# Kernel optimization log

Hardware: AMD Instinct MI355X
Metric: run time of the kernel (lower is better)

The kernel has to match this reference:

```python
import jax, jax.numpy as jnp
import numpy as np

EPS = 1e-5
K_PATCHES = 5000  # sample_pixels // 16


def _resize_bilinear(x, h, w):
    # matches torch F.interpolate(mode='bilinear', align_corners=False)
    return jax.image.resize(x, (x.shape[0], x.shape[1], h, w), method="bilinear", antialias=False)


def _bn(x, g, b, m, v):
    # eval-mode BatchNorm2d with running stats
    inv = jax.lax.rsqrt(v + EPS)
    return (x - m[None, :, None, None]) * (g * inv)[None, :, None, None] + b[None, :, None, None]


def _conv(x, w):
    return jax.lax.conv_general_dilated(x, w, (1, 1), "VALID",
                                        dimension_numbers=("NCHW", "OIHW", "NCHW"))


def setup_inputs():
    key = jax.random.key(0)
    ks = jax.random.split(key, 14)
    B, Hc, Wc = 2, 512, 512
    pha = jax.random.uniform(ks[0], (B, 1, Hc, Wc), jnp.float32)
    err = jax.random.uniform(ks[1], (B, 1, Hc, Wc), jnp.float32)  # strictly >0 so mask is all-ones
    hid = jax.random.normal(ks[2], (B, 32, Hc, Wc), jnp.float32)

    def conv_w(k, o, i):
        return jax.random.normal(k, (o, i, 3, 3), jnp.float32) * 0.05

    def bn_p(k, c):
        k1, k2 = jax.random.split(k)
        return (1.0 + 0.1 * jax.random.normal(k1, (c,), jnp.float32),
                0.1 * jax.random.normal(k2, (c,), jnp.float32),
                jnp.zeros((c,), jnp.float32), jnp.ones((c,), jnp.float32))

    g1, b1, m1, v1 = bn_p(ks[4], 24)
    g2, b2, m2, v2 = bn_p(ks[6], 16)
    g3, b3, m3, v3 = bn_p(ks[8], 12)
    return dict(pha=pha, err=err, hid=hid,
                w1=conv_w(ks[3], 24, 33), g1=g1, b1=b1, m1=m1, v1=v1,
                w2=conv_w(ks[5], 16, 24), g2=g2, b2=b2, m2=m2, v2=v2,
                w3=conv_w(ks[7], 12, 16), g3=g3, b3=b3, m3=m3, v3=v3,
                w4=conv_w(ks[9], 1, 12),
                b4=0.1 * jax.random.normal(ks[10], (1,), jnp.float32),
                H_full=2048, W_full=2048)


def reference(pha, err, hid, w1, g1, b1, m1, v1, w2, g2, b2, m2, v2,
              w3, g3, b3, m3, v3, w4, b4, H_full, W_full):
    B = pha.shape[0]
    Hh, Wh = H_full // 2, W_full // 2
    Hq, Wq = H_full // 4, W_full // 4

    # --- select_refinement_regions (sampling mode) ---
    err_q = _resize_bilinear(err, Hq, Wq)                      # (B,1,Hq,Wq)
    flat = err_q.reshape(B, -1)
    _, top_idx = jax.lax.top_k(flat, K_PATCHES)                # (B,K)
    ref = jnp.zeros_like(flat).at[jnp.arange(B)[:, None], top_idx].set(1.0)
    ref = ref * (flat > 0).astype(flat.dtype)                  # prevent_oversampling
    ref = ref.reshape(B, 1, Hq, Wq)

    # nonzero(ref) == topk locations here (err is strictly positive)
    bidx = jnp.repeat(jnp.arange(B), K_PATCHES)                # (P,)
    hidx = (top_idx // Wq).reshape(-1)                         # (P,)
    widx = (top_idx % Wq).reshape(-1)                          # (P,)

    # --- crop_patch (unfold-equivalent gather), size=2, padding=3 ---
    x = jnp.concatenate([hid, pha], axis=1)                    # (B,33,Hc,Wc)
    x = _resize_bilinear(x, Hh, Wh)                            # (B,33,Hh,Wh)
    pad, size = 3, 2
    win = size + 2 * pad                                       # 8
    xp = jnp.pad(x, ((0, 0), (0, 0), (pad, pad), (pad, pad)))
    rows = hidx[:, None] * size + jnp.arange(win)              # (P,8)
    cols = widx[:, None] * size + jnp.arange(win)              # (P,8)
    patches = xp[bidx[:, None, None], :, rows[:, :, None], cols[:, None, :]]  # (P,8,8,33)
    patches = patches.transpose(0, 3, 1, 2)                    # (P,33,8,8)

    # --- small conv stack ---
    y = jax.nn.relu(_bn(_conv(patches, w1), g1, b1, m1, v1))   # (P,24,6,6)
    y = jax.nn.relu(_bn(_conv(y, w2), g2, b2, m2, v2))         # (P,16,4,4)
    y = jnp.repeat(jnp.repeat(y, 2, axis=2), 2, axis=3)        # nearest -> (P,16,8,8)
    y = jax.nn.relu(_bn(_conv(y, w3), g3, b3, m3, v3))         # (P,12,6,6)
    y = _conv(y, w4) + b4[None, :, None, None]                 # (P,1,4,4)

    # --- replace_patch (scatter_nd of 4x4 blocks into full-res pha) ---
    pha_full = _resize_bilinear(pha, H_full, W_full)           # (B,1,H,W)
    pr = hidx[:, None, None] * 4 + jnp.arange(4)[None, :, None]  # (P,4,1)
    pc = widx[:, None, None] * 4 + jnp.arange(4)[None, None, :]  # (P,1,4)
    pha_full = pha_full.at[bidx[:, None, None], 0, pr, pc].set(y[:, 0])
    return pha_full, ref
```

## Files before the change

kernel.cpp:

```cpp
#include <hip/hip_runtime.h>
#include <stdint.h>

#define K_SEL 5000
#define NQ    262144
#define NB    2

#define BIAS_OFF 38912
#define W4_OFF   39424
#define ST_OFF   40960
#define XT_OFF   135168
#define XT_BYTES ((size_t)NB * NQ * 40 * 2)
#define WS_NEED  (XT_OFF + XT_BYTES)

#define WS_HIST  16
#define WS_SEL   2064
#define WS_EQ    12064
#define EQ_CAP   4096
#define WS_BCNT  20480

typedef _Float16 f16x8 __attribute__((ext_vector_type(8)));
typedef _Float16 f16x4 __attribute__((ext_vector_type(4)));
typedef float    f32x4 __attribute__((ext_vector_type(4)));
#define MFMA16(a,b,c) __builtin_amdgcn_mfma_f32_16x16x32_f16(a,b,c,0,0,0)

__global__ void prep_kernel(const float* __restrict__ w1, const float* __restrict__ g1,
                            const float* __restrict__ b1, const float* __restrict__ m1,
                            const float* __restrict__ v1,
                            const float* __restrict__ w2, const float* __restrict__ g2,
                            const float* __restrict__ b2, const float* __restrict__ m2,
                            const float* __restrict__ v2,
                            const float* __restrict__ w3, const float* __restrict__ g3,
                            const float* __restrict__ b3, const float* __restrict__ m3,
                            const float* __restrict__ v3,
                            const float* __restrict__ w4, const float* __restrict__ b4,
                            char* __restrict__ ws) {
    _Float16* wf = (_Float16*)ws;
    float* bias = (float*)(ws + BIAS_OFF);
    float* w4r  = (float*)(ws + W4_OFF);
    uint32_t* st = (uint32_t*)(ws + ST_OFF);
    int tid = threadIdx.x;
    for (int t = blockIdx.x * 256 + tid; t < 38 * 512; t += 64 * 256) {
        int frag = t >> 9, li = (t >> 3) & 63, j = t & 7;
        int lo = li & 15, hi = li >> 4;
        float val = 0.f;
        if (frag < 18) {
            int ky = frag / 6, r = frag % 6, kx = r >> 1, mt = r & 1;
            int oc = mt * 16 + lo, ci = hi * 8 + j;
            if (oc < 24) val = w1[((oc * 33 + ci) * 3 + ky) * 3 + kx] * g1[oc] * rsqrtf(v1[oc] + 1e-5f);
        } else if (frag < 27) {
            int f = frag - 18, ky = f / 3, kt = f % 3;
            int oc = lo, k = kt * 32 + hi * 8 + j;
            if (k < 72) {
                int kx = k / 24, ci = k % 24;
                val = w2[((oc * 24 + ci) * 3 + ky) * 3 + kx] * g2[oc] * rsqrtf(v2[oc] + 1e-5f);
            }
        } else if (frag < 36) {
            int s = frag - 27, ky = s / 3, kx = s % 3;
            int oc = lo, ci = hi * 8 + j;
            if (oc < 12 && ci < 16) val = w3[((oc * 16 + ci) * 3 + ky) * 3 + kx] * g3[oc] * rsqrtf(v3[oc] + 1e-5f);
        } else {
            int mt = frag - 36, oc = mt * 16 + lo, tap = hi * 8 + j;
            if (oc < 24 && tap < 9)
                val = w1[((oc * 33 + 32) * 3 + tap / 3) * 3 + tap % 3] * g1[oc] * rsqrtf(v1[oc] + 1e-5f);
        }
        wf[t] = (_Float16)val;
    }
    if (blockIdx.x == 0) {
        if (tid < 53) {
            float v;
            if (tid < 24)      { float sc = g1[tid] * rsqrtf(v1[tid] + 1e-5f); v = b1[tid] - m1[tid] * sc; }
            else if (tid < 40) { int c = tid - 24; float sc = g2[c] * rsqrtf(v2[c] + 1e-5f); v = b2[c] - m2[c] * sc; }
            else if (tid < 52) { int c = tid - 40; float sc = g3[c] * rsqrtf(v3[c] + 1e-5f); v = b3[c] - m3[c] * sc; }
            else v = b4[0];
            bias[tid] = v;
        }
        if (tid < 144) { int t9 = tid / 16, ci = tid % 16; w4r[tid] = (ci < 12) ? w4[ci * 9 + t9] : 0.f; }
        for (int i = tid; i < WS_HIST + 4 * 512; i += 256) st[i] = 0u;
    }
}

__device__ __forceinline__ void chain_scan(const uint32_t* __restrict__ st, int b, int nrounds,
                                           uint32_t* pref_out, uint32_t* rem_out) {
    int lane = threadIdx.x & 63;
    uint32_t pref = 0u, rem = K_SEL;
    for (int r = 0; r < nrounds; r++) {
        const uint32_t* hist = st + WS_HIST + r * 512 + b * 256;
        int binbase = 255 - 4 * lane;
        uint32_t hv0 = hist[binbase], hv1 = hist[binbase - 1],
                 hv2 = hist[binbase - 2], hv3 = hist[binbase - 3];
        uint32_t p = hv0 + hv1 + hv2 + hv3;
        uint32_t cum = p;
        for (int o = 1; o < 64; o <<= 1) {
            uint32_t n = __shfl_up(cum, o);
            if (lane >= o) cum += n;
        }
        unsigned long long bal = __ballot(cum >= rem);
        int first = __ffsll(bal) - 1;
        uint32_t acc = cum - p;
        uint32_t hv[4] = {hv0, hv1, hv2, hv3};
        int ch = binbase;
        for (int q = 0; q < 4; q++) {
            if (acc + hv[q] >= rem) { ch = binbase - q; break; }
            acc += hv[q];
        }
        uint32_t chosen = (uint32_t)__shfl((int)ch, first);
        uint32_t nrem   = (uint32_t)__shfl((int)(rem - acc), first);
        pref |= chosen << (24 - 8 * r);
        rem = nrem;
    }
    *pref_out = pref;
    *rem_out = rem;
}

__device__ __forceinline__ void tu_work(int tb, const float* __restrict__ hid,
                                        const float* __restrict__ pha,
                                        _Float16* __restrict__ xt,
                                        float* __restrict__ out) {
    int tid = threadIdx.x;
    if (tb < 2048) {
        int t = tb * 256 + tid;
        int b = t >> 18, i = t & (NQ - 1);
        _Float16 v[40];
#pragma unroll
        for (int c = 0; c < 32; c++)
            v[c] = (_Float16)hid[((size_t)(b * 32 + c)) * NQ + i];
        v[32] = (_Float16)pha[(size_t)b * NQ + i];
#pragma unroll
        for (int c = 33; c < 40; c++) v[c] = (_Float16)0.f;
        _Float16* dst = xt + (size_t)t * 40;
#pragma unroll
        for (int q = 0; q < 5; q++) *(f16x8*)(dst + q * 8) = *(const f16x8*)(v + q * 8);
    } else {
        int t = (tb - 2048) * 256 + tid;
        int xq = t & 511;
        int rest = t >> 9;
        int oy = rest & 2047;
        int b  = rest >> 11;
        const float* src = pha + (size_t)b * NQ;
        float sy = oy * 0.25f - 0.375f;
        sy = fminf(fmaxf(sy, 0.0f), 511.0f);
        int y0 = (int)sy; int y1i = min(y0 + 1, 511);
        float fy = sy - (float)y0;
        float rv[4];
#pragma unroll
        for (int j = 0; j < 4; j++) {
            int ox = xq * 4 + j;
            float sx = ox * 0.25f - 0.375f;
            sx = fminf(fmaxf(sx, 0.0f), 511.0f);
            int x0 = (int)sx; int x1i = min(x0 + 1, 511);
            float fx = sx - (float)x0;
            float v00 = src[y0 * 512 + x0],  v01 = src[y0 * 512 + x1i];
            float v10 = src[y1i * 512 + x0], v11 = src[y1i * 512 + x1i];
            rv[j] = v00 * (1.f - fy) * (1.f - fx) + v01 * (1.f - fy) * fx
                  + v10 * fy * (1.f - fx)         + v11 * fy * fx;
        }
        float4 r4 = make_float4(rv[0], rv[1], rv[2], rv[3]);
        *reinterpret_cast<float4*>(out + (size_t)b * 4194304 + (size_t)oy * 2048 + xq * 4) = r4;
    }
}

__global__ void upsample_kernel(const float* __restrict__ pha, float* __restrict__ out) {
    int t = blockIdx.x * 256 + threadIdx.x;
    int xq = t & 511;
    int rest = t >> 9;
    int oy = rest & 2047;
    int b  = rest >> 11;
    const float* src = pha + (size_t)b * NQ;
    float sy = oy * 0.25f - 0.375f;
    sy = fminf(fmaxf(sy, 0.0f), 511.0f);
    int y0 = (int)sy; int y1i = min(y0 + 1, 511);
    float fy = sy - (float)y0;
    float rv[4];
#pragma unroll
    for (int j = 0; j < 4; j++) {
        int ox = xq * 4 + j;
        float sx = ox * 0.25f - 0.375f;
        sx = fminf(fmaxf(sx, 0.0f), 511.0f);
        int x0 = (int)sx; int x1i = min(x0 + 1, 511);
        float fx = sx - (float)x0;
        float v00 = src[y0 * 512 + x0],  v01 = src[y0 * 512 + x1i];
        float v10 = src[y1i * 512 + x0], v11 = src[y1i * 512 + x1i];
        rv[j] = v00 * (1.f - fy) * (1.f - fx) + v01 * (1.f - fy) * fx
              + v10 * fy * (1.f - fx)         + v11 * fy * fx;
    }
    float4 r4 = make_float4(rv[0], rv[1], rv[2], rv[3]);
    *reinterpret_cast<float4*>(out + (size_t)b * 4194304 + (size_t)oy * 2048 + xq * 4) = r4;
}

__global__ void hist_kernel(const float* __restrict__ err, uint32_t* st, int round,
                            const float* __restrict__ hid, const float* __restrict__ pha,
                            _Float16* __restrict__ xt, float* __restrict__ out, int tu_base) {
    if (blockIdx.x >= 2048) { tu_work(blockIdx.x - 2048 + tu_base, hid, pha, xt, out); return; }
    __shared__ uint32_t h[256];
    h[threadIdx.x] = 0u;
    int t = blockIdx.x * 256 + threadIdx.x;
    int b = t >> 18;
    uint32_t pref = 0u, rem;
    if (round > 0) chain_scan(st, b, round, &pref, &rem);
    __syncthreads();
    uint32_t bits = __float_as_uint(err[t]);
    int shift = 24 - 8 * round;
    bool match = (round == 0) || ((bits >> (shift + 8)) == (pref >> (shift + 8)));
    if (match) atomicAdd(&h[(bits >> shift) & 255u], 1u);
    __syncthreads();
    uint32_t v = h[threadIdx.x];
    if (v) atomicAdd(&st[WS_HIST + round * 512 + b * 256 + threadIdx.x], v);
}

__global__ void ccount_kernel(const float* __restrict__ err, uint32_t* st,
                              const float* __restrict__ hid, const float* __restrict__ pha,
                              _Float16* __restrict__ xt, float* __restrict__ out, int tu_base) {
    if (blockIdx.x >= 1024) { tu_work(blockIdx.x - 1024 + tu_base, hid, pha, xt, out); return; }
    __shared__ uint32_t wsum[8];
    int blk = blockIdx.x, tid = threadIdx.x;
    int b = blk >> 9, base = (blk & 511) << 9;
    uint32_t T, need;
    chain_scan(st, b, 4, &T, &need);
    if ((blk & 511) == 0 && tid == 0) {
        atomicExch(&st[4 + b], T);
        atomicExch(&st[6 + b], need);
    }
    uint32_t b0 = __float_as_uint(err[b * NQ + base + tid]);
    uint32_t b1 = __float_as_uint(err[b * NQ + base + 256 + tid]);
    unsigned long long m0 = __ballot(b0 > T);
    unsigned long long m1 = __ballot(b1 > T);
    int w = tid >> 6, lane = tid & 63;
    if (lane == 0) { wsum[w] = (uint32_t)__popcll(m0); wsum[4 + w] = (uint32_t)__popcll(m1); }
    __syncthreads();
    if (tid == 0)
        st[WS_BCNT + blk] = wsum[0] + wsum[1] + wsum[2] + wsum[3]
                          + wsum[4] + wsum[5] + wsum[6] + wsum[7];
}

__global__ void cplace_kernel(const float* __restrict__ err, uint32_t* st,
                              float* __restrict__ refout,
                              const float* __restrict__ hid, const float* __restrict__ pha,
                              _Float16* __restrict__ xt, float* __restrict__ out, int tu_base) {
    if (blockIdx.x >= 1024) { tu_work(blockIdx.x - 1024 + tu_base, hid, pha, xt, out); return; }
    __shared__ uint32_t wc[8];
    __shared__ uint32_t red[4];
    int blk = blockIdx.x, tid = threadIdx.x;
    int b = blk >> 9, base = (blk & 511) << 9;
    int w = tid >> 6, lane = tid & 63;
    uint32_t T = st[4 + b];
    uint32_t myp = blk & 511;
    uint32_t c0 = st[WS_BCNT + b * 512 + 2 * tid];
    uint32_t c1 = st[WS_BCNT + b * 512 + 2 * tid + 1];
    uint32_t v = (((uint32_t)(2 * tid) < myp) ? c0 : 0u) + (((uint32_t)(2 * tid + 1) < myp) ? c1 : 0u);
    for (int o = 1; o < 64; o <<= 1) v += __shfl_xor(v, o);
    if (lane == 0) red[w] = v;
    __syncthreads();
    uint32_t blkbase = red[0] + red[1] + red[2] + red[3];
    if (myp == 511 && tid == 0)
        atomicExch(&st[8 + b], blkbase + st[WS_BCNT + b * 512 + 511]);
    int i0 = base + tid, i1 = base + 256 + tid;
    uint32_t b0 = __float_as_uint(err[b * NQ + i0]);
    uint32_t b1 = __float_as_uint(err[b * NQ + i1]);
    bool s0 = b0 > T, s1 = b1 > T;
    unsigned long long m0 = __ballot(s0);
    unsigned long long m1 = __ballot(s1);
    if (lane == 0) { wc[w] = (uint32_t)__popcll(m0); wc[4 + w] = (uint32_t)__popcll(m1); }
    refout[b * NQ + i0] = s0 ? 1.0f : 0.0f;
    refout[b * NQ + i1] = s1 ? 1.0f : 0.0f;
    __syncthreads();
    uint32_t tot0 = wc[0] + wc[1] + wc[2] + wc[3];
    uint32_t pre0 = 0, pre1 = tot0;
    for (int j = 0; j < w; j++) { pre0 += wc[j]; pre1 += wc[4 + j]; }
    unsigned long long lt = (1ull << lane) - 1ull;
    if (s0) {
        uint32_t slot = blkbase + pre0 + (uint32_t)__popcll(m0 & lt);
        if (slot < K_SEL) st[WS_SEL + b * K_SEL + slot] = (uint32_t)i0;
    }
    if (s1) {
        uint32_t slot = blkbase + pre1 + (uint32_t)__popcll(m1 & lt);
        if (slot < K_SEL) st[WS_SEL + b * K_SEL + slot] = (uint32_t)i1;
    }
    if (b0 == T) { uint32_t e = atomicAdd(&st[10 + b], 1u); if (e < EQ_CAP) st[WS_EQ + b * EQ_CAP + e] = (uint32_t)i0; }
    if (b1 == T) { uint32_t e = atomicAdd(&st[10 + b], 1u); if (e < EQ_CAP) st[WS_EQ + b * EQ_CAP + e] = (uint32_t)i1; }
}

__global__ void select_kernel(uint32_t* st, float* __restrict__ refout) {
    __shared__ uint32_t L[EQ_CAP];
    int b = blockIdx.x;
    uint32_t m = st[10 + b]; if (m > EQ_CAP) m = EQ_CAP;
    uint32_t need = st[6 + b];
    uint32_t T = st[4 + b];
    for (uint32_t j = threadIdx.x; j < m; j += blockDim.x) L[j] = st[WS_EQ + b * EQ_CAP + j];
    __syncthreads();
    for (uint32_t j = threadIdx.x; j < m; j += blockDim.x) {
        uint32_t idx = L[j];
        uint32_t rank = 0;
        for (uint32_t q = 0; q < m; q++) rank += (L[q] < idx) ? 1u : 0u;
        if (rank < need) {
            uint32_t slot = atomicAdd(&st[8 + b], 1u);
            if (slot < K_SEL) st[WS_SEL + b * K_SEL + slot] = idx;
            refout[b * NQ + idx] = (T != 0u) ? 1.0f : 0.0f;
        }
    }
}

__device__ __forceinline__ f16x8 ldfrag(const _Float16* wf, int frag, int l) {
    return *(const f16x8*)(wf + frag * 512 + l * 8);
}

template<bool XT>
__global__ __launch_bounds__(128) void patch_kernel(
    const float* __restrict__ hid, const float* __restrict__ pha,
    const _Float16* __restrict__ xt,
    const char* __restrict__ ws, float* __restrict__ out) {
    __shared__ _Float16 xs[64][40];
    __shared__ _Float16 y1n[36][40];
    __shared__ _Float16 pool[64][40];
    __shared__ float pha8[64];
    __shared__ float biasL[56];
    float* y3s = (float*)&y1n[0][0];

    const _Float16* wf = (const _Float16*)ws;
    const float* biasG = (const float*)(ws + BIAS_OFF);
    const float* w4r   = (const float*)(ws + W4_OFF);
    const uint32_t* st = (const uint32_t*)(ws + ST_OFF);

    int tid = threadIdx.x, l = tid & 63, wid = tid >> 6;
    int lo = l & 15, hi = l >> 4;
    int bp = blockIdx.x;
    int b = (bp >= K_SEL) ? 1 : 0;
    int pi = bp - b * K_SEL;
    uint32_t idx = st[WS_SEL + b * K_SEL + pi] & 0x3FFFFu;
    int hq = (int)(idx >> 9), wq = (int)(idx & 511u);

    if (tid < 53) biasL[tid] = biasG[tid];

    int ry = l >> 3, rx = l & 7;
    int hy = hq * 2 + ry - 3, hx = wq * 2 + rx - 3;
    bool inb = ((unsigned)hy < 1024u) && ((unsigned)hx < 1024u);
    float sy = fminf(fmaxf(hy * 0.5f - 0.25f, 0.f), 511.f);
    float sx = fminf(fmaxf(hx * 0.5f - 0.25f, 0.f), 511.f);
    int y0 = (int)sy, x0 = (int)sx;
    int y1c = min(y0 + 1, 511), x1c = min(x0 + 1, 511);
    float fy = sy - (float)y0, fx = sx - (float)x0;
    int o00 = y0 * 512 + x0, o01 = y0 * 512 + x1c, o10 = y1c * 512 + x0, o11 = y1c * 512 + x1c;
    float w00 = (1.f - fy) * (1.f - fx), w01 = (1.f - fy) * fx;
    float w10 = fy * (1.f - fx), w11 = fy * fx;

    _Float16 hv[16];
    if (XT) {
        if (inb) {
            const _Float16* xtb = xt + (size_t)b * NQ * 40 + (size_t)wid * 16;
            const _Float16* p00 = xtb + (size_t)o00 * 40;
            const _Float16* p01 = xtb + (size_t)o01 * 40;
            const _Float16* p10 = xtb + (size_t)o10 * 40;
            const _Float16* p11 = xtb + (size_t)o11 * 40;
            f16x8 a0 = *(const f16x8*)p00, a1 = *(const f16x8*)(p00 + 8);
            f16x8 b0 = *(const f16x8*)p01, b1 = *(const f16x8*)(p01 + 8);
            f16x8 c0 = *(const f16x8*)p10, c1 = *(const f16x8*)(p10 + 8);
            f16x8 d0 = *(const f16x8*)p11, d1 = *(const f16x8*)(p11 + 8);
#pragma unroll
            for (int j = 0; j < 8; j++) {
                hv[j]     = (_Float16)(w00 * (float)a0[j] + w01 * (float)b0[j]
                                     + w10 * (float)c0[j] + w11 * (float)d0[j]);
                hv[j + 8] = (_Float16)(w00 * (float)a1[j] + w01 * (float)b1[j]
                                     + w10 * (float)c1[j] + w11 * (float)d1[j]);
            }
        } else {
#pragma unroll
            for (int c = 0; c < 16; c++) hv[c] = (_Float16)0.f;
        }
    } else {
        const float* hb = hid + ((size_t)b * 32 + wid * 16) * NQ;
#pragma unroll
        for (int c = 0; c < 16; c++) {
            const float* p = hb + (size_t)c * NQ;
            float v = 0.f;
            if (inb) v = p[o00] * w00 + p[o01] * w01 + p[o10] * w10 + p[o11] * w11;
            hv[c] = (_Float16)v;
        }
    }
    f16x8 h0 = {hv[0], hv[1], hv[2], hv[3], hv[4], hv[5], hv[6], hv[7]};
    f16x8 h1 = {hv[8], hv[9], hv[10], hv[11], hv[12], hv[13], hv[14], hv[15]};
    {
        _Float16* xrow = &xs[l][wid * 16];
        *(f16x8*)xrow = h0;
        *((f16x8*)xrow + 1) = h1;
    }
    f16x8 z8 = {(_Float16)0.f, (_Float16)0.f, (_Float16)0.f, (_Float16)0.f,
                (_Float16)0.f, (_Float16)0.f, (_Float16)0.f, (_Float16)0.f};
    if (wid == 1) {
        const float* p = pha + (size_t)b * NQ;
        float v = 0.f;
        if (inb) v = p[o00] * w00 + p[o01] * w01 + p[o10] * w10 + p[o11] * w11;
        pha8[l] = v;
    }
    __syncthreads();

    if (wid == 0) {
        if (l < 48) {
            int py = (l * 43) >> 8, px = l - py * 6;
            _Float16 tap[9];
#pragma unroll
            for (int t = 0; t < 9; t++) {
                int ky = t / 3, kx = t % 3;
                int ip = (py + ky) * 8 + px + kx;
                tap[t] = (_Float16)pha8[ip & 63];
            }
            _Float16* row = &pool[l][0];
            f16x8 r0 = {tap[0], tap[1], tap[2], tap[3], tap[4], tap[5], tap[6], tap[7]};
            f16x8 r1 = z8; r1[0] = tap[8];
            *(f16x8*)row = r0;
            *(f16x8*)(row + 8)  = r1;
            *(f16x8*)(row + 16) = z8;
            *(f16x8*)(row + 24) = z8;
        }
    } else {
        for (int i = l; i < 72; i += 64) {
            *(f16x8*)&y1n[i >> 1][24 + (i & 1) * 8] = z8;
        }
    }
    __syncthreads();

    f32x4 zf = {0.f, 0.f, 0.f, 0.f};
    f32x4 aA0 = zf, aA1 = zf, aB = zf;
    int nA = wid * 16 + lo, nB = 32 + lo;
    int pyA = (nA * 43) >> 8, pxA = nA - pyA * 6;
    int pyB = (nB * 43) >> 8, pxB = nB - pyB * 6;
    {
        f16x8 A0 = ldfrag(wf, 36, l), A1 = ldfrag(wf, 37, l);
        f16x8 BA = *(const f16x8*)&pool[nA][hi * 8];
        f16x8 BB = *(const f16x8*)&pool[nB][hi * 8];
        aA0 = MFMA16(A0, BA, aA0);
        aA1 = MFMA16(A1, BA, aA1);
        aB  = MFMA16(wid ? A1 : A0, BB, aB);
    }
#pragma unroll
    for (int ky = 0; ky < 3; ky++) {
#pragma unroll
        for (int kt = 0; kt < 3; kt++) {
            f16x8 A0 = ldfrag(wf, ky * 6 + kt * 2 + 0, l);
            f16x8 A1 = ldfrag(wf, ky * 6 + kt * 2 + 1, l);
            int rA = ((pyA + ky) * 8 + pxA + kt) & 63;
            int rB = ((pyB + ky) * 8 + pxB + kt) & 63;
            f16x8 BA = *(const f16x8*)&xs[rA][hi * 8];
            f16x8 BB = *(const f16x8*)&xs[rB][hi * 8];
            aA0 = MFMA16(A0, BA, aA0);
            aA1 = MFMA16(A1, BA, aA1);
            aB  = MFMA16(wid ? A1 : A0, BB, aB);
        }
    }
    {
        f32x4 accs[3] = {aA0, aA1, aB};
        int mts[3] = {0, 1, wid};
        int nts[3] = {wid, wid, 2};
#pragma unroll
        for (int f = 0; f < 3; f++) {
            int n = nts[f] * 16 + lo;
            int ocb = mts[f] * 16 + hi * 4;
            if (n < 36 && ocb < 24) {
                f16x4 hh;
                hh[0] = (_Float16)fmaxf(accs[f][0] + biasL[ocb + 0], 0.f);
                hh[1] = (_Float16)fmaxf(accs[f][1] + biasL[ocb + 1], 0.f);
                hh[2] = (_Float16)fmaxf(accs[f][2] + biasL[ocb + 2], 0.f);
                hh[3] = (_Float16)fmaxf(accs[f][3] + biasL[ocb + 3], 0.f);
                *(f16x4*)&y1n[n][ocb] = hh;
            }
        }
    }
    __syncthreads();

    if (wid == 0) {
        f32x4 a2 = zf;
        int qy = lo >> 2, qx = lo & 3;
#pragma unroll
        for (int ky = 0; ky < 3; ky++) {
#pragma unroll
            for (int kt = 0; kt < 3; kt++) {
                f16x8 A = ldfrag(wf, 18 + ky * 3 + kt, l);
                int k = kt * 32 + hi * 8;
                const _Float16* bptr;
                if (k < 72) {
                    int kx = k / 24, ci0 = k - kx * 24;
                    bptr = &y1n[(qy + ky) * 6 + qx + kx][ci0];
                } else {
                    bptr = &y1n[0][24];
                }
                f16x8 B = *(const f16x8*)bptr;
                a2 = MFMA16(A, B, a2);
            }
        }
        int ocb = hi * 4;
        f16x4 hh;
        hh[0] = (_Float16)fmaxf(a2[0] + biasL[24 + ocb + 0], 0.f);
        hh[1] = (_Float16)fmaxf(a2[1] + biasL[24 + ocb + 1], 0.f);
        hh[2] = (_Float16)fmaxf(a2[2] + biasL[24 + ocb + 2], 0.f);
        hh[3] = (_Float16)fmaxf(a2[3] + biasL[24 + ocb + 3], 0.f);
#pragma unroll
        for (int dy = 0; dy < 2; dy++)
#pragma unroll
            for (int dx = 0; dx < 2; dx++) {
                int row = (2 * qy + dy) * 8 + 2 * qx + dx;
                *(f16x4*)&pool[row][ocb] = hh;
            }
    } else {
        *(f16x8*)&pool[l][16] = z8;
        *(f16x8*)&pool[l][24] = z8;
    }
    __syncthreads();

    f32x4 aC = zf, aD = zf;
    int nC = wid * 16 + lo, nD = 32 + lo;
    int pyC = (nC * 43) >> 8, pxC = nC - pyC * 6;
    int pyD = (nD * 43) >> 8, pxD = nD - pyD * 6;
#pragma unroll
    for (int s = 0; s < 9; s++) {
        int ky = s / 3, kx = s % 3;
        f16x8 A = ldfrag(wf, 27 + s, l);
        f16x8 BC = *(const f16x8*)&pool[((pyC + ky) * 8 + pxC + kx) & 63][hi * 8];
        aC = MFMA16(A, BC, aC);
        if (wid) {
            f16x8 BD = *(const f16x8*)&pool[((pyD + ky) * 8 + pxD + kx) & 63][hi * 8];
            aD = MFMA16(A, BD, aD);
        }
    }
    __syncthreads();
    {
        int ocb = hi * 4;
        f32x4 accs[2] = {aC, aD};
        int nts[2] = {wid, 2};
        int cnt = wid ? 2 : 1;
        for (int f = 0; f < cnt; f++) {
            int n = nts[f] * 16 + lo;
            if (n < 36) {
                f32x4 v;
#pragma unroll
                for (int r = 0; r < 4; r++) {
                    float bb = (ocb + r < 12) ? biasL[40 + ocb + r] : 0.f;
                    float x = accs[f][r] + bb;
                    v[r] = (ocb + r < 12) ? fmaxf(x, 0.f) : 0.f;
                }
                *(f32x4*)&y3s[n * 16 + ocb] = v;
            }
        }
    }
    __syncthreads();

    if (wid == 0) {
        int r4 = lo >> 2, c4 = lo & 3, cig = hi;
        float acc = 0.f;
#pragma unroll
        for (int t = 0; t < 9; t++) {
            int ky = t / 3, kx = t % 3;
            const f32x4 xv = *(const f32x4*)&y3s[((r4 + ky) * 6 + c4 + kx) * 16 + cig * 4];
            const f32x4 wv = *(const f32x4*)(w4r + t * 16 + cig * 4);
            acc += xv[0] * wv[0] + xv[1] * wv[1] + xv[2] * wv[2] + xv[3] * wv[3];
        }
        acc += __shfl_xor(acc, 32);
        acc += __shfl_xor(acc, 16);
        if (l < 16) {
            out[(size_t)b * 4194304 + (size_t)(hq * 4 + r4) * 2048 + (wq * 4 + c4)] = acc + biasL[52];
        }
    }
}

extern "C" void kernel_launch(void* const* d_in, const int* in_sizes, int n_in,
                              void* d_out, int out_size, void* d_ws, size_t ws_size,
                              hipStream_t stream) {
    const float* pha = (const float*)d_in[0];
    const float* err = (const float*)d_in[1];
    const float* hid = (const float*)d_in[2];
    const float* w1  = (const float*)d_in[3];
    const float* g1  = (const float*)d_in[4];
    const float* bb1 = (const float*)d_in[5];
    const float* m1  = (const float*)d_in[6];
    const float* v1  = (const float*)d_in[7];
    const float* w2  = (const float*)d_in[8];
    const float* g2  = (const float*)d_in[9];
    const float* bb2 = (const float*)d_in[10];
    const float* m2  = (const float*)d_in[11];
    const float* v2  = (const float*)d_in[12];
    const float* w3  = (const float*)d_in[13];
    const float* g3  = (const float*)d_in[14];
    const float* bb3 = (const float*)d_in[15];
    const float* m3  = (const float*)d_in[16];
    const float* v3  = (const float*)d_in[17];
    const float* w4  = (const float*)d_in[18];
    const float* b4  = (const float*)d_in[19];

    float* out    = (float*)d_out;
    float* refout = out + (size_t)NB * 4194304;
    char* ws      = (char*)d_ws;
    uint32_t* st  = (uint32_t*)(ws + ST_OFF);
    _Float16* xt  = (_Float16*)(ws + XT_OFF);
    bool use_xt   = (ws_size >= WS_NEED);

    prep_kernel<<<64, 256, 0, stream>>>(w1, g1, bb1, m1, v1, w2, g2, bb2, m2, v2,
                                        w3, g3, bb3, m3, v3, w4, b4, ws);
    if (use_xt) {
        const int NTU = 10240, SLICE = 1707;
        int off = 0;
        for (int r = 0; r < 4; r++) {
            int n = (off + SLICE <= NTU) ? SLICE : (NTU - off);
            hist_kernel<<<2048 + n, 256, 0, stream>>>(err, st, r, hid, pha, xt, out, off);
            off += n;
        }
        {
            int n = (off + SLICE <= NTU) ? SLICE : (NTU - off);
            ccount_kernel<<<1024 + n, 256, 0, stream>>>(err, st, hid, pha, xt, out, off);
            off += n;
        }
        {
            int n = NTU - off;
            cplace_kernel<<<1024 + n, 256, 0, stream>>>(err, st, refout, hid, pha, xt, out, off);
        }
        select_kernel<<<2, 256, 0, stream>>>(st, refout);
        patch_kernel<true><<<2 * K_SEL, 128, 0, stream>>>(hid, pha, xt, ws, out);
    } else {
        upsample_kernel<<<8192, 256, 0, stream>>>(pha, out);
        for (int r = 0; r < 4; r++)
            hist_kernel<<<2048, 256, 0, stream>>>(err, st, r, hid, pha, xt, out, 0);
        ccount_kernel<<<1024, 256, 0, stream>>>(err, st, hid, pha, xt, out, 0);
        cplace_kernel<<<1024, 256, 0, stream>>>(err, st, refout, hid, pha, xt, out, 0);
        select_kernel<<<2, 256, 0, stream>>>(st, refout);
        patch_kernel<false><<<2 * K_SEL, 128, 0, stream>>>(hid, pha, xt, ws, out);
    }
}
```

Baseline: 136.7 us.

## Remove select kernel via deterministic tie ranking and merge prep into first histogram

Ties at the threshold are now ranked with per-block prefix counts in ccount and cplace, replacing the atomic equal-list plus the O(m^2) single-block select_kernel. The weight-prep work is folded into the first radix-histogram launch, and state zeroing moves to a hipMemsetAsync. This removes two kernel launches and a serial tail stage, at the cost of packing both counts into 16-bit halves of one word, which assumes each count fits in 16 bits.

```diff
diff --git a/kernel.cpp b/kernel.cpp
--- a/kernel.cpp
+++ b/kernel.cpp
@@ -14,8 +14,6 @@
 
 #define WS_HIST  16
 #define WS_SEL   2064
-#define WS_EQ    12064
-#define EQ_CAP   4096
 #define WS_BCNT  20480
 
 typedef _Float16 f16x8 __attribute__((ext_vector_type(8)));
@@ -23,23 +21,23 @@
 typedef float    f32x4 __attribute__((ext_vector_type(4)));
 #define MFMA16(a,b,c) __builtin_amdgcn_mfma_f32_16x16x32_f16(a,b,c,0,0,0)
 
-__global__ void prep_kernel(const float* __restrict__ w1, const float* __restrict__ g1,
-                            const float* __restrict__ b1, const float* __restrict__ m1,
-                            const float* __restrict__ v1,
-                            const float* __restrict__ w2, const float* __restrict__ g2,
-                            const float* __restrict__ b2, const float* __restrict__ m2,
-                            const float* __restrict__ v2,
-                            const float* __restrict__ w3, const float* __restrict__ g3,
-                            const float* __restrict__ b3, const float* __restrict__ m3,
-                            const float* __restrict__ v3,
-                            const float* __restrict__ w4, const float* __restrict__ b4,
-                            char* __restrict__ ws) {
+__device__ void prep_work(int bid,
+                          const float* __restrict__ w1, const float* __restrict__ g1,
+                          const float* __restrict__ b1, const float* __restrict__ m1,
+                          const float* __restrict__ v1,
+                          const float* __restrict__ w2, const float* __restrict__ g2,
+                          const float* __restrict__ b2, const float* __restrict__ m2,
+                          const float* __restrict__ v2,
+                          const float* __restrict__ w3, const float* __restrict__ g3,
+                          const float* __restrict__ b3, const float* __restrict__ m3,
+                          const float* __restrict__ v3,
+                          const float* __restrict__ w4, const float* __restrict__ b4,
+                          char* __restrict__ ws) {
     _Float16* wf = (_Float16*)ws;
     float* bias = (float*)(ws + BIAS_OFF);
     float* w4r  = (float*)(ws + W4_OFF);
-    uint32_t* st = (uint32_t*)(ws + ST_OFF);
     int tid = threadIdx.x;
-    for (int t = blockIdx.x * 256 + tid; t < 38 * 512; t += 64 * 256) {
+    for (int t = bid * 256 + tid; t < 38 * 512; t += 64 * 256) {
         int frag = t >> 9, li = (t >> 3) & 63, j = t & 7;
         int lo = li & 15, hi = li >> 4;
         float val = 0.f;
@@ -65,7 +63,7 @@
         }
         wf[t] = (_Float16)val;
     }
-    if (blockIdx.x == 0) {
+    if (bid == 0) {
         if (tid < 53) {
             float v;
             if (tid < 24)      { float sc = g1[tid] * rsqrtf(v1[tid] + 1e-5f); v = b1[tid] - m1[tid] * sc; }
@@ -75,7 +73,6 @@
             bias[tid] = v;
         }
         if (tid < 144) { int t9 = tid / 16, ci = tid % 16; w4r[tid] = (ci < 12) ? w4[ci * 9 + t9] : 0.f; }
-        for (int i = tid; i < WS_HIST + 4 * 512; i += 256) st[i] = 0u;
     }
 }
 
@@ -187,6 +184,40 @@
     *reinterpret_cast<float4*>(out + (size_t)b * 4194304 + (size_t)oy * 2048 + xq * 4) = r4;
 }
 
+__global__ void l1_kernel(const float* __restrict__ err, uint32_t* st,
+                          const float* __restrict__ w1, const float* __restrict__ g1,
+                          const float* __restrict__ b1, const float* __restrict__ m1,
+                          const float* __restrict__ v1,
+                          const float* __restrict__ w2, const float* __restrict__ g2,
+                          const float* __restrict__ b2, const float* __restrict__ m2,
+                          const float* __restrict__ v2,
+                          const float* __restrict__ w3, const float* __restrict__ g3,
+                          const float* __restrict__ b3, const float* __restrict__ m3,
+                          const float* __restrict__ v3,
+                          const float* __restrict__ w4, const float* __restrict__ b4,
+                          char* __restrict__ ws,
+                          const float* __restrict__ hid, const float* __restrict__ pha,
+                          _Float16* __restrict__ xt, float* __restrict__ out, int tu_base) {
+    int blk = blockIdx.x, tid = threadIdx.x;
+    if (blk < 2048) {
+        __shared__ uint32_t h[256];
+        h[tid] = 0u;
+        __syncthreads();
+        int t = blk * 256 + tid;
+        int b = t >> 18;
+        uint32_t bits = __float_as_uint(err[t]);
+        atomicAdd(&h[bits >> 24], 1u);
+        __syncthreads();
+        uint32_t v = h[tid];
+        if (v) atomicAdd(&st[WS_HIST + b * 256 + tid], v);
+    } else if (blk < 2112) {
+        prep_work(blk - 2048, w1, g1, b1, m1, v1, w2, g2, b2, m2, v2,
+                  w3, g3, b3, m3, v3, w4, b4, ws);
+    } else {
+        tu_work(blk - 2112 + tu_base, hid, pha, xt, out);
+    }
+}
+
 __global__ void hist_kernel(const float* __restrict__ err, uint32_t* st, int round,
                             const float* __restrict__ hid, const float* __restrict__ pha,
                             _Float16* __restrict__ xt, float* __restrict__ out, int tu_base) {
@@ -195,12 +226,12 @@
     h[threadIdx.x] = 0u;
     int t = blockIdx.x * 256 + threadIdx.x;
     int b = t >> 18;
-    uint32_t pref = 0u, rem;
-    if (round > 0) chain_scan(st, b, round, &pref, &rem);
+    uint32_t pref, rem;
+    chain_scan(st, b, round, &pref, &rem);
     __syncthreads();
     uint32_t bits = __float_as_uint(err[t]);
     int shift = 24 - 8 * round;
-    bool match = (round == 0) || ((bits >> (shift + 8)) == (pref >> (shift + 8)));
+    bool match = ((bits >> (shift + 8)) == (pref >> (shift + 8)));
     if (match) atomicAdd(&h[(bits >> shift) & 255u], 1u);
     __syncthreads();
     uint32_t v = h[threadIdx.x];
@@ -211,7 +242,7 @@
                               const float* __restrict__ hid, const float* __restrict__ pha,
                               _Float16* __restrict__ xt, float* __restrict__ out, int tu_base) {
     if (blockIdx.x >= 1024) { tu_work(blockIdx.x - 1024 + tu_base, hid, pha, xt, out); return; }
-    __shared__ uint32_t wsum[8];
+    __shared__ uint32_t wsum[16];
     int blk = blockIdx.x, tid = threadIdx.x;
     int b = blk >> 9, base = (blk & 511) << 9;
     uint32_t T, need;
@@ -222,14 +253,21 @@
     }
     uint32_t b0 = __float_as_uint(err[b * NQ + base + tid]);
     uint32_t b1 = __float_as_uint(err[b * NQ + base + 256 + tid]);
-    unsigned long long m0 = __ballot(b0 > T);
-    unsigned long long m1 = __ballot(b1 > T);
+    unsigned long long m0s = __ballot(b0 > T), m1s = __ballot(b1 > T);
+    unsigned long long m0e = __ballot(b0 == T), m1e = __ballot(b1 == T);
     int w = tid >> 6, lane = tid & 63;
-    if (lane == 0) { wsum[w] = (uint32_t)__popcll(m0); wsum[4 + w] = (uint32_t)__popcll(m1); }
-    __syncthreads();
-    if (tid == 0)
-        st[WS_BCNT + blk] = wsum[0] + wsum[1] + wsum[2] + wsum[3]
-                          + wsum[4] + wsum[5] + wsum[6] + wsum[7];
+    if (lane == 0) {
+        wsum[w]      = (uint32_t)__popcll(m0s);
+        wsum[4 + w]  = (uint32_t)__popcll(m1s);
+        wsum[8 + w]  = (uint32_t)__popcll(m0e);
+        wsum[12 + w] = (uint32_t)__popcll(m1e);
+    }
+    __syncthreads();
+    if (tid == 0) {
+        uint32_t s = 0, e = 0;
+        for (int j = 0; j < 8; j++) { s += wsum[j]; e += wsum[8 + j]; }
+        st[WS_BCNT + blk] = s | (e << 16);
+    }
 }
 
 __global__ void cplace_kernel(const float* __restrict__ err, uint32_t* st,
@@ -237,66 +275,79 @@
                               const float* __restrict__ hid, const float* __restrict__ pha,
                               _Float16* __restrict__ xt, float* __restrict__ out, int tu_base) {
     if (blockIdx.x >= 1024) { tu_work(blockIdx.x - 1024 + tu_base, hid, pha, xt, out); return; }
-    __shared__ uint32_t wc[8];
-    __shared__ uint32_t red[4];
+    __shared__ uint32_t wcS[8], wcE[8];
+    __shared__ uint32_t redP[4], redE[4];
     int blk = blockIdx.x, tid = threadIdx.x;
     int b = blk >> 9, base = (blk & 511) << 9;
     int w = tid >> 6, lane = tid & 63;
     uint32_t T = st[4 + b];
+    uint32_t need = st[6 + b];
     uint32_t myp = blk & 511;
-    uint32_t c0 = st[WS_BCNT + b * 512 + 2 * tid];
-    uint32_t c1 = st[WS_BCNT + b * 512 + 2 * tid + 1];
-    uint32_t v = (((uint32_t)(2 * tid) < myp) ? c0 : 0u) + (((uint32_t)(2 * tid + 1) < myp) ? c1 : 0u);
-    for (int o = 1; o < 64; o <<= 1) v += __shfl_xor(v, o);
-    if (lane == 0) red[w] = v;
-    __syncthreads();
-    uint32_t blkbase = red[0] + red[1] + red[2] + red[3];
-    if (myp == 511 && tid == 0)
-        atomicExch(&st[8 + b], blkbase + st[WS_BCNT + b * 512 + 511]);
+    uint32_t p0 = st[WS_BCNT + b * 512 + 2 * tid];
+    uint32_t p1 = st[WS_BCNT + b * 512 + 2 * tid + 1];
+    uint32_t s0c = p0 & 0xFFFFu, s1c = p1 & 0xFFFFu;
+    uint32_t e0c = p0 >> 16,     e1c = p1 >> 16;
+    uint32_t vP = (((uint32_t)(2 * tid) < myp) ? s0c : 0u)
+                + (((uint32_t)(2 * tid + 1) < myp) ? s1c : 0u)
+                + ((s0c + s1c) << 16);
+    uint32_t vE = (((uint32_t)(2 * tid) < myp) ? e0c : 0u)
+                + (((uint32_t)(2 * tid + 1) < myp) ? e1c : 0u);
+    for (int o = 1; o < 64; o <<= 1) { vP += __shfl_xor(vP, o); vE += __shfl_xor(vE, o); }
+    if (lane == 0) { redP[w] = vP; redE[w] = vE; }
+    __syncthreads();
+    uint32_t sumP = redP[0] + redP[1] + redP[2] + redP[3];
+    uint32_t eqbase   = redE[0] + redE[1] + redE[2] + redE[3];
+    uint32_t selbase  = sumP & 0xFFFFu;
+    uint32_t selTotal = sumP >> 16;
+
     int i0 = base + tid, i1 = base + 256 + tid;
     uint32_t b0 = __float_as_uint(err[b * NQ + i0]);
     uint32_t b1 = __float_as_uint(err[b * NQ + i1]);
     bool s0 = b0 > T, s1 = b1 > T;
-    unsigned long long m0 = __ballot(s0);
-    unsigned long long m1 = __ballot(s1);
-    if (lane == 0) { wc[w] = (uint32_t)__popcll(m0); wc[4 + w] = (uint32_t)__popcll(m1); }
-    refout[b * NQ + i0] = s0 ? 1.0f : 0.0f;
-    refout[b * NQ + i1] = s1 ? 1.0f : 0.0f;
-    __syncthreads();
-    uint32_t tot0 = wc[0] + wc[1] + wc[2] + wc[3];
-    uint32_t pre0 = 0, pre1 = tot0;
-    for (int j = 0; j < w; j++) { pre0 += wc[j]; pre1 += wc[4 + j]; }
+    bool q0 = b0 == T, q1 = b1 == T;
+    unsigned long long m0s = __ballot(s0), m1s = __ballot(s1);
+    unsigned long long m0e = __ballot(q0), m1e = __ballot(q1);
+    if (lane == 0) {
+        wcS[w] = (uint32_t)__popcll(m0s); wcS[4 + w] = (uint32_t)__popcll(m1s);
+        wcE[w] = (uint32_t)__popcll(m0e); wcE[4 + w] = (uint32_t)__popcll(m1e);
+    }
+    __syncthreads();
+    uint32_t tot0S = wcS[0] + wcS[1] + wcS[2] + wcS[3];
+    uint32_t tot0E = wcE[0] + wcE[1] + wcE[2] + wcE[3];
+    uint32_t preS0 = 0, preS1 = tot0S, preE0 = 0, preE1 = tot0E;
+    for (int j = 0; j < w; j++) {
+        preS0 += wcS[j]; preS1 += wcS[4 + j];
+        preE0 += wcE[j]; preE1 += wcE[4 + j];
+    }
     unsigned long long lt = (1ull << lane) - 1ull;
+    float rv0 = s0 ? 1.0f : 0.0f;
+    float rv1 = s1 ? 1.0f : 0.0f;
     if (s0) {
-        uint32_t slot = blkbase + pre0 + (uint32_t)__popcll(m0 & lt);
+        uint32_t slot = selbase + preS0 + (uint32_t)__popcll(m0s & lt);
         if (slot < K_SEL) st[WS_SEL + b * K_SEL + slot] = (uint32_t)i0;
     }
     if (s1) {
-        uint32_t slot = blkbase + pre1 + (uint32_t)__popcll(m1 & lt);
+        uint32_t slot = selbase + preS1 + (uint32_t)__popcll(m1s & lt);
         if (slot < K_SEL) st[WS_SEL + b * K_SEL + slot] = (uint32_t)i1;
     }
-    if (b0 == T) { uint32_t e = atomicAdd(&st[10 + b], 1u); if (e < EQ_CAP) st[WS_EQ + b * EQ_CAP + e] = (uint32_t)i0; }
-    if (b1 == T) { uint32_t e = atomicAdd(&st[10 + b], 1u); if (e < EQ_CAP) st[WS_EQ + b * EQ_CAP + e] = (uint32_t)i1; }
-}
-
-__global__ void select_kernel(uint32_t* st, float* __restrict__ refout) {
-    __shared__ uint32_t L[EQ_CAP];
-    int b = blockIdx.x;
-    uint32_t m = st[10 + b]; if (m > EQ_CAP) m = EQ_CAP;
-    uint32_t need = st[6 + b];
-    uint32_t T = st[4 + b];
-    for (uint32_t j = threadIdx.x; j < m; j += blockDim.x) L[j] = st[WS_EQ + b * EQ_CAP + j];
-    __syncthreads();
-    for (uint32_t j = threadIdx.x; j < m; j += blockDim.x) {
-        uint32_t idx = L[j];
-        uint32_t rank = 0;
-        for (uint32_t q = 0; q < m; q++) rank += (L[q] < idx) ? 1u : 0u;
+    if (q0) {
+        uint32_t rank = eqbase + preE0 + (uint32_t)__popcll(m0e & lt);
         if (rank < need) {
-            uint32_t slot = atomicAdd(&st[8 + b], 1u);
-            if (slot < K_SEL) st[WS_SEL + b * K_SEL + slot] = idx;
-            refout[b * NQ + idx] = (T != 0u) ? 1.0f : 0.0f;
-        }
-    }
+            uint32_t slot = selTotal + rank;
+            if (slot < K_SEL) st[WS_SEL + b * K_SEL + slot] = (uint32_t)i0;
+            rv0 = (T != 0u) ? 1.0f : 0.0f;
+        }
+    }
+    if (q1) {
+        uint32_t rank = eqbase + preE1 + (uint32_t)__popcll(m1e & lt);
+        if (rank < need) {
+            uint32_t slot = selTotal + rank;
+            if (slot < K_SEL) st[WS_SEL + b * K_SEL + slot] = (uint32_t)i1;
+            rv1 = (T != 0u) ? 1.0f : 0.0f;
+        }
+    }
+    refout[b * NQ + i0] = rv0;
+    refout[b * NQ + i1] = rv1;
 }
 
 __device__ __forceinline__ f16x8 ldfrag(const _Float16* wf, int frag, int l) {
@@ -590,34 +641,36 @@
     _Float16* xt  = (_Float16*)(ws + XT_OFF);
     bool use_xt   = (ws_size >= WS_NEED);
 
-    prep_kernel<<<64, 256, 0, stream>>>(w1, g1, bb1, m1, v1, w2, g2, bb2, m2, v2,
-                                        w3, g3, bb3, m3, v3, w4, b4, ws);
+    hipMemsetAsync(st, 0, (WS_HIST + 4 * 512) * sizeof(uint32_t), stream);
+
     if (use_xt) {
         const int NTU = 10240, SLICE = 1707;
         int off = 0;
-        for (int r = 0; r < 4; r++) {
-            int n = (off + SLICE <= NTU) ? SLICE : (NTU - off);
+        int n = SLICE;
+        l1_kernel<<<2112 + n, 256, 0, stream>>>(err, st, w1, g1, bb1, m1, v1,
+                                                w2, g2, bb2, m2, v2, w3, g3, bb3, m3, v3,
+                                                w4, b4, ws, hid, pha, xt, out, off);
+        off += n;
+        for (int r = 1; r < 4; r++) {
+            n = (off + SLICE <= NTU) ? SLICE : (NTU - off);
             hist_kernel<<<2048 + n, 256, 0, stream>>>(err, st, r, hid, pha, xt, out, off);
             off += n;
         }
-        {
-            int n = (off + SLICE <= NTU) ? SLICE : (NTU - off);
-            ccount_kernel<<<1024 + n, 256, 0, stream>>>(err, st, hid, pha, xt, out, off);
-            off += n;
-        }
-        {
-            int n = NTU - off;
-            cplace_kernel<<<1024 + n, 256, 0, stream>>>(err, st, refout, hid, pha, xt, out, off);
-        }
-        select_kernel<<<2, 256, 0, stream>>>(st, refout);
+        n = (off + SLICE <= NTU) ? SLICE : (NTU - off);
+        ccount_kernel<<<1024 + n, 256, 0, stream>>>(err, st, hid, pha, xt, out, off);
+        off += n;
+        n = NTU - off;
+        cplace_kernel<<<1024 + n, 256, 0, stream>>>(err, st, refout, hid, pha, xt, out, off);
         patch_kernel<true><<<2 * K_SEL, 128, 0, stream>>>(hid, pha, xt, ws, out);
     } else {
         upsample_kernel<<<8192, 256, 0, stream>>>(pha, out);
-        for (int r = 0; r < 4; r++)
+        l1_kernel<<<2112, 256, 0, stream>>>(err, st, w1, g1, bb1, m1, v1,
+                                            w2, g2, bb2, m2, v2, w3, g3, bb3, m3, v3,
+                                            w4, b4, ws, hid, pha, xt, out, 0);
+        for (int r = 1; r < 4; r++)
             hist_kernel<<<2048, 256, 0, stream>>>(err, st, r, hid, pha, xt, out, 0);
         ccount_kernel<<<1024, 256, 0, stream>>>(err, st, hid, pha, xt, out, 0);
         cplace_kernel<<<1024, 256, 0, stream>>>(err, st, refout, hid, pha, xt, out, 0);
-        select_kernel<<<2, 256, 0, stream>>>(st, refout);
         patch_kernel<false><<<2 * K_SEL, 128, 0, stream>>>(hid, pha, xt, ws, out);
     }
 }
```

New measurement: 135.5 us (median of 2 runs). Within noise of the previous version (-0.9%).
